# Kernel optimization log

Hardware: AMD Instinct MI355X
Metric: run time of the kernel (lower is better)

## Reference

```python
import jax, jax.numpy as jnp
import numpy as np

D_MODEL = 512; D_INNER = 1024; D_STATE = 16; D_CONV = 4; DT_RANK = 32
MRI_DIM = 1024; CLIN_DIM = 64; N_SLICES = 2000; CHUNK = 500; N_LAYERS = 3; N_HEADS = 8


def _ln(x, g, b, eps=1e-5):
    m = x.mean(-1, keepdims=True)
    v = ((x - m) ** 2).mean(-1, keepdims=True)
    return (x - m) / jnp.sqrt(v + eps) * g + b


def _mamba(x, in_proj, conv_w, conv_b, x_proj, dt_w, dt_b, A_log, Dp, out_proj):
    # x: (B, L, d_model). Faithful mamba-ssm block (no biases on in/out proj).
    B, L, _ = x.shape
    xz = jnp.einsum('bld,ed->ble', x, in_proj)          # (B, L, 2*d_inner)
    xr, z = jnp.split(xz, 2, axis=-1)
    # depthwise causal conv1d, kernel D_CONV, truncated to seqlen
    xp = jnp.pad(xr, ((0, 0), (D_CONV - 1, 0), (0, 0)))
    xc = sum(conv_w[:, k] * xp[:, k:k + L, :] for k in range(D_CONV)) + conv_b
    xc = jax.nn.silu(xc)                                # (B, L, d_inner)
    proj = jnp.einsum('bld,ed->ble', xc, x_proj)        # (B, L, dt_rank+2*d_state)
    dt_in = proj[..., :DT_RANK]
    Bm = proj[..., DT_RANK:DT_RANK + D_STATE]
    Cm = proj[..., DT_RANK + D_STATE:]
    dt = jax.nn.softplus(jnp.einsum('blr,dr->bld', dt_in, dt_w) + dt_b)  # (B, L, d_inner)
    A = -jnp.exp(A_log)                                 # (d_inner, d_state)
    dA = jnp.exp(dt[..., None] * A)                     # (B, L, d_inner, d_state)
    dBx = dt[..., None] * Bm[:, :, None, :] * xc[..., None]

    def step(h, inp):
        dA_t, dBx_t, C_t = inp
        h = dA_t * h + dBx_t
        return h, jnp.einsum('bds,bs->bd', h, C_t)

    h0 = jnp.zeros((B, D_INNER, D_STATE), x.dtype)
    _, ys = jax.lax.scan(step, h0, (dA.transpose(1, 0, 2, 3), dBx.transpose(1, 0, 2, 3), Cm.transpose(1, 0, 2)))
    y = ys.transpose(1, 0, 2) + Dp * xc
    y = y * jax.nn.silu(z)
    return jnp.einsum('ble,de->bld', y, out_proj)


def _mha(q, k, v, in_w, in_b, out_w, out_b, nh):
    # torch nn.MultiheadAttention (batch_first), returns (out, head-averaged weights)
    E = q.shape[-1]; hd = E // nh
    wq, wk, wv = jnp.split(in_w, 3, axis=0)
    bq, bk, bv = jnp.split(in_b, 3, axis=0)
    Q = (q @ wq.T + bq).reshape(q.shape[0], q.shape[1], nh, hd)
    K = (k @ wk.T + bk).reshape(k.shape[0], k.shape[1], nh, hd)
    V = (v @ wv.T + bv).reshape(v.shape[0], v.shape[1], nh, hd)
    s = jnp.einsum('blhd,bshd->bhls', Q, K) / jnp.sqrt(jnp.asarray(hd, q.dtype))
    a = jax.nn.softmax(s, axis=-1)
    o = jnp.einsum('bhls,bshd->blhd', a, V).reshape(q.shape[0], q.shape[1], E)
    return o @ out_w.T + out_b, a.mean(axis=1)


def setup_inputs() -> dict:
    key = jax.random.key(0)
    ks = iter(jax.random.split(key, 100))
    def rnd(shape, s=0.02):
        return s * jax.random.normal(next(ks), shape, jnp.float32)
    d = {}
    d['slice_features'] = jax.random.normal(next(ks), (N_SLICES, MRI_DIM), jnp.float32)
    d['clinical_features'] = jax.random.normal(next(ks), (CLIN_DIM,), jnp.float32)
    d['enc_in_W'] = rnd((D_MODEL, MRI_DIM)); d['enc_in_b'] = jnp.zeros((D_MODEL,))
    d['enc_in_ln_g'] = jnp.ones((D_MODEL,)); d['enc_in_ln_b'] = jnp.zeros((D_MODEL,))
    def mamba_params(n):
        return dict(
            in_proj=rnd((n, 2 * D_INNER, D_MODEL)),
            conv_w=rnd((n, D_INNER, D_CONV), 0.1),
            conv_b=jnp.zeros((n, D_INNER)),
            x_proj=rnd((n, DT_RANK + 2 * D_STATE, D_INNER)),
            dt_w=rnd((n, D_INNER, DT_RANK), 0.1),
            dt_b=jnp.full((n, D_INNER), -4.6, jnp.float32),  # softplus ~ 0.01
            A_log=jnp.log(jnp.broadcast_to(jnp.arange(1, D_STATE + 1, dtype=jnp.float32), (n, D_INNER, D_STATE))),
            D=jnp.ones((n, D_INNER)),
            out_proj=rnd((n, D_MODEL, D_INNER)))
    for k2, v in mamba_params(2).items():
        d['em_' + k2] = v
    d['enc_ln_g'] = jnp.ones((2, D_MODEL)); d['enc_ln_b'] = jnp.zeros((2, D_MODEL))
    d['enc_out_W'] = rnd((D_MODEL, D_MODEL)); d['enc_out_b'] = jnp.zeros((D_MODEL,))
    d['cl_w1'] = rnd((64, CLIN_DIM)); d['cl_b1'] = jnp.zeros((64,))
    d['cl_ln1_g'] = jnp.ones((64,)); d['cl_ln1_b'] = jnp.zeros((64,))
    d['cl_w2'] = rnd((D_MODEL, 64)); d['cl_b2'] = jnp.zeros((D_MODEL,))
    d['cl_ln2_g'] = jnp.ones((D_MODEL,)); d['cl_ln2_b'] = jnp.zeros((D_MODEL,))
    for k2, v in mamba_params(N_LAYERS).items():
        d['lm_' + k2] = v
    d['l_mln_g'] = jnp.ones((N_LAYERS, D_MODEL)); d['l_mln_b'] = jnp.zeros((N_LAYERS, D_MODEL))
    d['ca_in_w'] = rnd((N_LAYERS, 3 * D_MODEL, D_MODEL)); d['ca_in_b'] = jnp.zeros((N_LAYERS, 3 * D_MODEL))
    d['ca_out_w'] = rnd((N_LAYERS, D_MODEL, D_MODEL)); d['ca_out_b'] = jnp.zeros((N_LAYERS, D_MODEL))
    d['ca_ln_g'] = jnp.ones((N_LAYERS, D_MODEL)); d['ca_ln_b'] = jnp.zeros((N_LAYERS, D_MODEL))
    d['ff_w1'] = rnd((N_LAYERS, 2 * D_MODEL, D_MODEL)); d['ff_b1'] = jnp.zeros((N_LAYERS, 2 * D_MODEL))
    d['ff_w2'] = rnd((N_LAYERS, D_MODEL, 2 * D_MODEL)); d['ff_b2'] = jnp.zeros((N_LAYERS, D_MODEL))
    d['ffn_ln_g'] = jnp.ones((N_LAYERS, D_MODEL)); d['ffn_ln_b'] = jnp.zeros((N_LAYERS, D_MODEL))
    d['agg_in_w'] = rnd((3 * D_MODEL, D_MODEL)); d['agg_in_b'] = jnp.zeros((3 * D_MODEL,))
    d['agg_out_w'] = rnd((D_MODEL, D_MODEL)); d['agg_out_b'] = jnp.zeros((D_MODEL,))
    d['op_w'] = rnd((64, D_MODEL)); d['op_b'] = jnp.zeros((64,))
    d['op_ln_g'] = jnp.ones((64,)); d['op_ln_b'] = jnp.zeros((64,))
    return d


def reference(slice_features, clinical_features, enc_in_W, enc_in_b, enc_in_ln_g, enc_in_ln_b,
              em_in_proj, em_conv_w, em_conv_b, em_x_proj, em_dt_w, em_dt_b, em_A_log, em_D, em_out_proj,
              enc_ln_g, enc_ln_b, enc_out_W, enc_out_b,
              cl_w1, cl_b1, cl_ln1_g, cl_ln1_b, cl_w2, cl_b2, cl_ln2_g, cl_ln2_b,
              lm_in_proj, lm_conv_w, lm_conv_b, lm_x_proj, lm_dt_w, lm_dt_b, lm_A_log, lm_D, lm_out_proj,
              l_mln_g, l_mln_b, ca_in_w, ca_in_b, ca_out_w, ca_out_b, ca_ln_g, ca_ln_b,
              ff_w1, ff_b1, ff_w2, ff_b2, ffn_ln_g, ffn_ln_b,
              agg_in_w, agg_in_b, agg_out_w, agg_out_b, op_w, op_b, op_ln_g, op_ln_b):
    # --- MRI slice encoder: chunks of 500 slices, each a Mamba sequence (batched over chunks) ---
    h = slice_features.reshape(N_SLICES // CHUNK, CHUNK, MRI_DIM)
    h = _ln(h @ enc_in_W.T + enc_in_b, enc_in_ln_g, enc_in_ln_b)
    for i in range(2):
        res = h
        h = _mamba(h, em_in_proj[i], em_conv_w[i], em_conv_b[i], em_x_proj[i],
                   em_dt_w[i], em_dt_b[i], em_A_log[i], em_D[i], em_out_proj[i])
        h = _ln(h + res, enc_ln_g[i], enc_ln_b[i])
    mri = (h @ enc_out_W.T + enc_out_b).reshape(N_SLICES, D_MODEL)
    mri = jax.lax.stop_gradient(mri)  # .detach() in the original
    # --- clinical encoder ---
    c = jax.nn.relu(_ln(cl_w1 @ clinical_features + cl_b1, cl_ln1_g, cl_ln1_b))
    c = jax.nn.relu(_ln(cl_w2 @ c + cl_b2, cl_ln2_g, cl_ln2_b))
    seq = mri[None]                 # (1, N, D)
    cseq = c.reshape(1, 1, D_MODEL)
    # --- MambaFormer cross-attention layers ---
    for i in range(N_LAYERS):
        res = seq
        m = _mamba(seq, lm_in_proj[i], lm_conv_w[i], lm_conv_b[i], lm_x_proj[i],
                   lm_dt_w[i], lm_dt_b[i], lm_A_log[i], lm_D[i], lm_out_proj[i])
        seq = _ln(m + res, l_mln_g[i], l_mln_b[i])
        att, _ = _mha(seq, cseq, cseq, ca_in_w[i], ca_in_b[i], ca_out_w[i], ca_out_b[i], N_HEADS)
        seq = _ln(att + seq, ca_ln_g[i], ca_ln_b[i])
        f = jax.nn.gelu(seq @ ff_w1[i].T + ff_b1[i], approximate=False) @ ff_w2[i].T + ff_b2[i]
        seq = _ln(f + seq, ffn_ln_g[i], ffn_ln_b[i])
    # --- attention aggregation ---
    agg, w = _mha(seq, seq, seq, agg_in_w, agg_in_b, agg_out_w, agg_out_b, N_HEADS)
    scores = w.mean(axis=1)[0]                      # (N,): mean over query dim of head-avg weights
    emb = jnp.sum(scores[:, None] * agg[0], axis=0)  # (D,)
    return jax.nn.relu(_ln(op_w @ emb + op_b, op_ln_g, op_ln_b))
```

## Files before the change

kernel.cpp:

```cpp
#include <hip/hip_runtime.h>
#include <hip/hip_bf16.h>

#define NSL 2000
#define DM 512
#define DI 1024
#define DS 16
#define DTR 32

enum {
  IN_SLICE=0, IN_CLIN, IN_ENC_IN_W, IN_ENC_IN_B, IN_ENC_IN_LN_G, IN_ENC_IN_LN_B,
  IN_EM_IN_PROJ, IN_EM_CONV_W, IN_EM_CONV_B, IN_EM_X_PROJ, IN_EM_DT_W, IN_EM_DT_B,
  IN_EM_A_LOG, IN_EM_D, IN_EM_OUT_PROJ, IN_ENC_LN_G, IN_ENC_LN_B, IN_ENC_OUT_W, IN_ENC_OUT_B,
  IN_CL_W1, IN_CL_B1, IN_CL_LN1_G, IN_CL_LN1_B, IN_CL_W2, IN_CL_B2, IN_CL_LN2_G, IN_CL_LN2_B,
  IN_LM_IN_PROJ, IN_LM_CONV_W, IN_LM_CONV_B, IN_LM_X_PROJ, IN_LM_DT_W, IN_LM_DT_B,
  IN_LM_A_LOG, IN_LM_D, IN_LM_OUT_PROJ, IN_L_MLN_G, IN_L_MLN_B,
  IN_CA_IN_W, IN_CA_IN_B, IN_CA_OUT_W, IN_CA_OUT_B, IN_CA_LN_G, IN_CA_LN_B,
  IN_FF_W1, IN_FF_B1, IN_FF_W2, IN_FF_B2, IN_FFN_LN_G, IN_FFN_LN_B,
  IN_AGG_IN_W, IN_AGG_IN_B, IN_AGG_OUT_W, IN_AGG_OUT_B,
  IN_OP_W, IN_OP_B, IN_OP_LN_G, IN_OP_LN_B
};

typedef __attribute__((ext_vector_type(8))) __bf16 bf16x8;
typedef __attribute__((ext_vector_type(4))) float f32x4;
typedef __attribute__((ext_vector_type(8))) unsigned short u16x8;

__device__ __forceinline__ float softplusf_(float x) {
  return (x > 15.f) ? x : __logf(1.f + __expf(x));
}
__device__ __forceinline__ float siluf_(float x) {
  return x / (1.f + __expf(-x));
}
__device__ __forceinline__ unsigned short f2bf(float f) {
  unsigned int u = __float_as_uint(f);
  u += 0x7fff + ((u >> 16) & 1);
  return (unsigned short)(u >> 16);
}

#define NCVT 13
struct CvtArgs {
  const float* s[NCVT];
  unsigned short* d[NCVT];
  int n[NCVT];
};
__global__ __launch_bounds__(256) void cvt_batch(CvtArgs a) {
  const int ti = blockIdx.y;
  const int base = (blockIdx.x * 256 + threadIdx.x) * 16;
  if (base >= a.n[ti]) return;
  const float* s = a.s[ti];
  unsigned short* d = a.d[ti];
#pragma unroll
  for (int q = 0; q < 4; ++q) {
    float4 v = *reinterpret_cast<const float4*>(s + base + q * 4);
    ushort4 u; u.x = f2bf(v.x); u.y = f2bf(v.y); u.z = f2bf(v.z); u.w = f2bf(v.w);
    *reinterpret_cast<ushort4*>(d + base + q * 4) = u;
  }
}

template<int BM, int BN, int EPI>
__global__ __launch_bounds__(256) void gemm_mfma(
    const unsigned short* __restrict__ A, int lda,
    const unsigned short* __restrict__ W, int ldw,
    const float* __restrict__ bias,
    float* __restrict__ C, unsigned short* __restrict__ C16, int ldc,
    int M, int N, int K)
{
  constexpr int LS = 72;
  __shared__ unsigned short Als[BM][LS];
  __shared__ unsigned short Wls[BN][LS];
  constexpr int TPRA = 256 / BM;
  constexpr int USA  = 64 / TPRA;
  constexpr int TPRW = 256 / BN;
  constexpr int USW  = 64 / TPRW;
  constexpr int FM = BM / 32, FN = BN / 32;

  const int tid  = threadIdx.x;
  const int m0   = blockIdx.y * BM, n0 = blockIdx.x * BN;
  const int wave = tid >> 6, lane = tid & 63;
  const int wm   = wave >> 1, wn = wave & 1;
  const int lrow = lane & 15, lgrp = lane >> 4;

  f32x4 acc[FM][FN];
#pragma unroll
  for (int i = 0; i < FM; ++i)
#pragma unroll
    for (int j = 0; j < FN; ++j) acc[i][j] = (f32x4){0.f, 0.f, 0.f, 0.f};

  const int sra = tid / TPRA, ska = (tid % TPRA) * USA;
  const int srw = tid / TPRW, skw = (tid % TPRW) * USW;
  const int gma = m0 + sra;
  const int gnw = n0 + srw;

  for (int k0 = 0; k0 < K; k0 += 64) {
#pragma unroll
    for (int f = 0; f < USA / 8; ++f) {
      u16x8 v = {0,0,0,0,0,0,0,0};
      if (gma < M) v = *reinterpret_cast<const u16x8*>(&A[(size_t)gma * lda + k0 + ska + 8 * f]);
      *reinterpret_cast<u16x8*>(&Als[sra][ska + 8 * f]) = v;
    }
#pragma unroll
    for (int f = 0; f < USW / 8; ++f) {
      u16x8 v = {0,0,0,0,0,0,0,0};
      if (gnw < N) v = *reinterpret_cast<const u16x8*>(&W[(size_t)gnw * ldw + k0 + skw + 8 * f]);
      *reinterpret_cast<u16x8*>(&Wls[srw][skw + 8 * f]) = v;
    }
    __syncthreads();
#pragma unroll
    for (int ks = 0; ks < 2; ++ks) {
      bf16x8 am[FM], bn[FN];
#pragma unroll
      for (int i = 0; i < FM; ++i)
        am[i] = *reinterpret_cast<const bf16x8*>(&Als[wm * (BM / 2) + i * 16 + lrow][ks * 32 + lgrp * 8]);
#pragma unroll
      for (int j = 0; j < FN; ++j)
        bn[j] = *reinterpret_cast<const bf16x8*>(&Wls[wn * (BN / 2) + j * 16 + lrow][ks * 32 + lgrp * 8]);
#pragma unroll
      for (int i = 0; i < FM; ++i)
#pragma unroll
        for (int j = 0; j < FN; ++j)
          acc[i][j] = __builtin_amdgcn_mfma_f32_16x16x32_bf16(am[i], bn[j], acc[i][j], 0, 0, 0);
    }
    __syncthreads();
  }

#pragma unroll
  for (int i = 0; i < FM; ++i) {
#pragma unroll
    for (int j = 0; j < FN; ++j) {
#pragma unroll
      for (int q = 0; q < 4; ++q) {
        int gm = m0 + wm * (BM / 2) + i * 16 + lgrp * 4 + q;
        int gn = n0 + wn * (BN / 2) + j * 16 + lrow;
        if (gm < M && gn < N) {
          float v = acc[i][j][q];
          if (bias) v += bias[gn];
          if (EPI == 1) v = 0.5f * v * (1.f + erff(v * 0.70710678118654752f));
          if (C)   C[(size_t)gm * ldc + gn] = v;
          if (C16) C16[(size_t)gm * ldc + gn] = f2bf(v);
        }
      }
    }
  }
}

__global__ __launch_bounds__(256) void ln512_kernel(
    const float* __restrict__ x, const float* __restrict__ res,
    const float* __restrict__ g, const float* __restrict__ b,
    float* __restrict__ out, unsigned short* __restrict__ out16)
{
  const int row = blockIdx.x, tid = threadIdx.x;
  const size_t base = (size_t)row * 512;
  float v0 = x[base + tid], v1 = x[base + tid + 256];
  if (res) { v0 += res[base + tid];  v1 += res[base + tid + 256]; }
  float s = v0 + v1, ss = v0*v0 + v1*v1;
#pragma unroll
  for (int off = 1; off < 64; off <<= 1) {
    s  += __shfl_xor(s,  off);
    ss += __shfl_xor(ss, off);
  }
  __shared__ float rs[4], rss[4];
  int wid = tid >> 6, lane = tid & 63;
  if (lane == 0) { rs[wid] = s; rss[wid] = ss; }
  __syncthreads();
  s  = rs[0] + rs[1] + rs[2] + rs[3];
  ss = rss[0] + rss[1] + rss[2] + rss[3];
  float mean = s * (1.f/512.f);
  float var  = ss * (1.f/512.f) - mean*mean;
  float rstd = rsqrtf(var + 1e-5f);
  float o0 = g[tid]     * (v0 - mean) * rstd + b[tid];
  float o1 = g[tid+256] * (v1 - mean) * rstd + b[tid+256];
  out[base + tid]       = o0;
  out[base + tid + 256] = o1;
  if (out16) {
    out16[base + tid]       = f2bf(o0);
    out16[base + tid + 256] = f2bf(o1);
  }
}

__global__ __launch_bounds__(256) void ln512_dual(
    const float* __restrict__ x, const float* __restrict__ res,
    const float* __restrict__ addvec,
    const float* __restrict__ g1, const float* __restrict__ b1,
    const float* __restrict__ g2, const float* __restrict__ b2,
    float* __restrict__ out, unsigned short* __restrict__ out16)
{
  const int row = blockIdx.x, tid = threadIdx.x;
  const size_t base = (size_t)row * 512;
  __shared__ float rs[4], rss[4];
  int wid = tid >> 6, lane = tid & 63;

  float v0 = x[base + tid] + res[base + tid];
  float v1 = x[base + tid + 256] + res[base + tid + 256];
  float s = v0 + v1, ss = v0*v0 + v1*v1;
#pragma unroll
  for (int off = 1; off < 64; off <<= 1) { s += __shfl_xor(s, off); ss += __shfl_xor(ss, off); }
  if (lane == 0) { rs[wid] = s; rss[wid] = ss; }
  __syncthreads();
  s  = rs[0] + rs[1] + rs[2] + rs[3];
  ss = rss[0] + rss[1] + rss[2] + rss[3];
  float mean = s * (1.f/512.f);
  float rstd = rsqrtf(ss * (1.f/512.f) - mean*mean + 1e-5f);
  float u0 = g1[tid]     * (v0 - mean) * rstd + b1[tid]     + addvec[tid];
  float u1 = g1[tid+256] * (v1 - mean) * rstd + b1[tid+256] + addvec[tid+256];

  float s2 = u0 + u1, ss2 = u0*u0 + u1*u1;
#pragma unroll
  for (int off = 1; off < 64; off <<= 1) { s2 += __shfl_xor(s2, off); ss2 += __shfl_xor(ss2, off); }
  __syncthreads();
  if (lane == 0) { rs[wid] = s2; rss[wid] = ss2; }
  __syncthreads();
  s2  = rs[0] + rs[1] + rs[2] + rs[3];
  ss2 = rss[0] + rss[1] + rss[2] + rss[3];
  float mean2 = s2 * (1.f/512.f);
  float rstd2 = rsqrtf(ss2 * (1.f/512.f) - mean2*mean2 + 1e-5f);
  float o0 = g2[tid]     * (u0 - mean2) * rstd2 + b2[tid];
  float o1 = g2[tid+256] * (u1 - mean2) * rstd2 + b2[tid+256];
  out[base + tid]       = o0;
  out[base + tid + 256] = o1;
  out16[base + tid]       = f2bf(o0);
  out16[base + tid + 256] = f2bf(o1);
}

__global__ __launch_bounds__(256) void conv_silu_kernel(
    const float* __restrict__ xz, const float* __restrict__ cw,
    const float* __restrict__ cb, float* __restrict__ xc,
    unsigned short* __restrict__ xc16, int L)
{
  int idx = blockIdx.x * 256 + threadIdx.x;
  if (idx >= NSL * DI) return;
  int rrow = idx >> 10, c = idx & 1023;
  int l = rrow % L;
  float acc = cb[c];
  const float w0 = cw[c*4+0], w1 = cw[c*4+1], w2 = cw[c*4+2], w3 = cw[c*4+3];
  const float* base = xz + (size_t)rrow * 2048 + c;
  if (l >= 3) acc += w0 * base[-3*2048];
  if (l >= 2) acc += w1 * base[-2*2048];
  if (l >= 1) acc += w2 * base[-1*2048];
  acc += w3 * base[0];
  float r = siluf_(acc);
  xc[idx] = r;
  xc16[idx] = f2bf(r);
}

__global__ __launch_bounds__(256) void scan_p1(
    const float* __restrict__ proj, const float* __restrict__ dt_w,
    const float* __restrict__ dt_b, const float* __restrict__ xc,
    float* __restrict__ Pb, float* __restrict__ Eb, int L, int T)
{
  const int lane = threadIdx.x & 63, wave = threadIdx.x >> 6;
  const int dl = wave * 32 + (lane & 31);
  const int shalf = lane >> 5;
  const int d = blockIdx.x * 128 + dl;
  const int c = blockIdx.y, b = blockIdx.z, B = gridDim.z;
  const int s0 = shalf * 8;

  float dtw[32];
#pragma unroll
  for (int q = 0; q < 8; ++q)
    *reinterpret_cast<float4*>(&dtw[q*4]) = *reinterpret_cast<const float4*>(&dt_w[(size_t)d * 32 + q * 4]);
  const float dtbv = dt_b[d];

  float h[8];
#pragma unroll
  for (int s = 0; s < 8; ++s) h[s] = 0.f;
  float R = 1.f;

  int t0 = c * T, t1 = t0 + T; if (t1 > L) t1 = L;
  for (int t = t0; t < t1; ++t) {
    size_t row = (size_t)b * L + t;
    const float* pr = proj + row * 64;
    float dacc = dtbv;
#pragma unroll
    for (int q = 0; q < 8; ++q) {
      float4 p4 = *reinterpret_cast<const float4*>(pr + q * 4);
      dacc = fmaf(p4.x, dtw[q*4+0], dacc);
      dacc = fmaf(p4.y, dtw[q*4+1], dacc);
      dacc = fmaf(p4.z, dtw[q*4+2], dacc);
      dacc = fmaf(p4.w, dtw[q*4+3], dacc);
    }
    float dtv = softplusf_(dacc);
    float r1 = __expf(-dtv);
    float xcv = xc[row * 1024 + d];
    float u = dtv * xcv;
    float4 b0 = *reinterpret_cast<const float4*>(pr + 32 + s0);
    float4 b1 = *reinterpret_cast<const float4*>(pr + 36 + s0);
    float r2 = r1 * r1, r4 = r2 * r2, r8 = r4 * r4;
    float rp = shalf ? (r8 * r1) : r1;
    h[0] = fmaf(rp, h[0], u * b0.x); rp *= r1;
    h[1] = fmaf(rp, h[1], u * b0.y); rp *= r1;
    h[2] = fmaf(rp, h[2], u * b0.z); rp *= r1;
    h[3] = fmaf(rp, h[3], u * b0.w); rp *= r1;
    h[4] = fmaf(rp, h[4], u * b1.x); rp *= r1;
    h[5] = fmaf(rp, h[5], u * b1.y); rp *= r1;
    h[6] = fmaf(rp, h[6], u * b1.z); rp *= r1;
    h[7] = fmaf(rp, h[7], u * b1.w);
    R *= r1;
  }
  float R2 = R * R, R4 = R2 * R2, R8 = R4 * R4;
  float Rp = shalf ? (R8 * R) : R;
  float P[8];
  P[0] = Rp; Rp *= R; P[1] = Rp; Rp *= R; P[2] = Rp; Rp *= R; P[3] = Rp; Rp *= R;
  P[4] = Rp; Rp *= R; P[5] = Rp; Rp *= R; P[6] = Rp; Rp *= R; P[7] = Rp;
  size_t o = (((size_t)(c * B + b)) << 14) + (size_t)d * 16 + s0;
  *reinterpret_cast<float4*>(&Pb[o])     = (float4){P[0], P[1], P[2], P[3]};
  *reinterpret_cast<float4*>(&Pb[o + 4]) = (float4){P[4], P[5], P[6], P[7]};
  *reinterpret_cast<float4*>(&Eb[o])     = (float4){h[0], h[1], h[2], h[3]};
  *reinterpret_cast<float4*>(&Eb[o + 4]) = (float4){h[4], h[5], h[6], h[7]};
}

__global__ __launch_bounds__(256) void scan_comb(
    const float* __restrict__ Pb, const float* __restrict__ Eb,
    float* __restrict__ Gb, int B, int nC)
{
  int idx = blockIdx.x * 256 + threadIdx.x;
  if (idx >= B * 16384) return;
  int b = idx >> 14, ds = idx & 16383;
  float gacc = 0.f;
#pragma unroll 4
  for (int c = 0; c < nC; ++c) {
    size_t o = (((size_t)(c * B + b)) << 14) + ds;
    Gb[o] = gacc;
    gacc = fmaf(Pb[o], gacc, Eb[o]);
  }
}

__global__ __launch_bounds__(256) void scan_p3(
    const float* __restrict__ proj, const float* __restrict__ dt_w,
    const float* __restrict__ dt_b, const float* __restrict__ xc,
    const float* __restrict__ xz, const float* __restrict__ Dp,
    const float* __restrict__ Gb, unsigned short* __restrict__ y16, int L, int T)
{
  const int lane = threadIdx.x & 63, wave = threadIdx.x >> 6;
  const int dl = wave * 32 + (lane & 31);
  const int shalf = lane >> 5;
  const int d = blockIdx.x * 128 + dl;
  const int c = blockIdx.y, b = blockIdx.z, B = gridDim.z;
  const int s0 = shalf * 8;

  float dtw[32];
#pragma unroll
  for (int q = 0; q < 8; ++q)
    *reinterpret_cast<float4*>(&dtw[q*4]) = *reinterpret_cast<const float4*>(&dt_w[(size_t)d * 32 + q * 4]);
  const float dtbv = dt_b[d];
  const float Dv = Dp[d];

  size_t o = (((size_t)(c * B + b)) << 14) + (size_t)d * 16 + s0;
  float4 g0 = *reinterpret_cast<const float4*>(&Gb[o]);
  float4 g1 = *reinterpret_cast<const float4*>(&Gb[o + 4]);
  float h[8] = {g0.x, g0.y, g0.z, g0.w, g1.x, g1.y, g1.z, g1.w};

  int t0 = c * T, t1 = t0 + T; if (t1 > L) t1 = L;
  for (int t = t0; t < t1; ++t) {
    size_t row = (size_t)b * L + t;
    const float* pr = proj + row * 64;
    float dacc = dtbv;
#pragma unroll
    for (int q = 0; q < 8; ++q) {
      float4 p4 = *reinterpret_cast<const float4*>(pr + q * 4);
      dacc = fmaf(p4.x, dtw[q*4+0], dacc);
      dacc = fmaf(p4.y, dtw[q*4+1], dacc);
      dacc = fmaf(p4.z, dtw[q*4+2], dacc);
      dacc = fmaf(p4.w, dtw[q*4+3], dacc);
    }
    float dtv = softplusf_(dacc);
    float r1 = __expf(-dtv);
    float xcv = xc[row * 1024 + d];
    float u = dtv * xcv;
    float4 b0 = *reinterpret_cast<const float4*>(pr + 32 + s0);
    float4 b1 = *reinterpret_cast<const float4*>(pr + 36 + s0);
    float4 c0 = *reinterpret_cast<const float4*>(pr + 48 + s0);
    float4 c1 = *reinterpret_cast<const float4*>(pr + 52 + s0);
    float r2 = r1 * r1, r4 = r2 * r2, r8 = r4 * r4;
    float rp = shalf ? (r8 * r1) : r1;
    float yv;
    h[0] = fmaf(rp, h[0], u * b0.x); yv  = h[0] * c0.x; rp *= r1;
    h[1] = fmaf(rp, h[1], u * b0.y); yv = fmaf(h[1], c0.y, yv); rp *= r1;
    h[2] = fmaf(rp, h[2], u * b0.z); yv = fmaf(h[2], c0.z, yv); rp *= r1;
    h[3] = fmaf(rp, h[3], u * b0.w); yv = fmaf(h[3], c0.w, yv); rp *= r1;
    h[4] = fmaf(rp, h[4], u * b1.x); yv = fmaf(h[4], c1.x, yv); rp *= r1;
    h[5] = fmaf(rp, h[5], u * b1.y); yv = fmaf(h[5], c1.y, yv); rp *= r1;
    h[6] = fmaf(rp, h[6], u * b1.z); yv = fmaf(h[6], c1.z, yv); rp *= r1;
    h[7] = fmaf(rp, h[7], u * b1.w); yv = fmaf(h[7], c1.w, yv);
    yv += __shfl_xor(yv, 32);
    if (shalf == 0) {
      float zv = xz[row * 2048 + 1024 + d];
      y16[row * 1024 + d] = f2bf((yv + Dv * xcv) * siluf_(zv));
    }
  }
}

__global__ __launch_bounds__(512) void clinical_kernel(
    const float* __restrict__ clin,
    const float* __restrict__ w1, const float* __restrict__ b1,
    const float* __restrict__ g1, const float* __restrict__ bb1,
    const float* __restrict__ w2, const float* __restrict__ b2,
    const float* __restrict__ g2, const float* __restrict__ bb2,
    float* __restrict__ c2out)
{
  __shared__ float cs[64], c1[64], red[16];
  const int tid = threadIdx.x;
  if (tid < 64) cs[tid] = clin[tid];
  __syncthreads();
  if (tid < 64) {
    float a1 = b1[tid];
    for (int k = 0; k < 64; ++k) a1 = fmaf(w1[tid*64 + k], cs[k], a1);
    float s = a1, ss = a1*a1;
#pragma unroll
    for (int off = 1; off < 64; off <<= 1) { s += __shfl_xor(s, off); ss += __shfl_xor(ss, off); }
    float m = s * (1.f/64.f), var = ss * (1.f/64.f) - m*m;
    float r = rsqrtf(var + 1e-5f);
    float v = g1[tid] * (a1 - m) * r + bb1[tid];
    c1[tid] = fmaxf(v, 0.f);
  }
  __syncthreads();
  float a2 = b2[tid];
  for (int k = 0; k < 64; ++k) a2 = fmaf(w2[tid*64 + k], c1[k], a2);
  float s = a2, ss = a2*a2;
#pragma unroll
  for (int off = 1; off < 64; off <<= 1) { s += __shfl_xor(s, off); ss += __shfl_xor(ss, off); }
  int wid = tid >> 6, lane = tid & 63;
  if (lane == 0) { red[wid] = s; red[8 + wid] = ss; }
  __syncthreads();
  s = 0.f; ss = 0.f;
#pragma unroll
  for (int q = 0; q < 8; ++q) { s += red[q]; ss += red[8+q]; }
  float m = s * (1.f/512.f), var = ss * (1.f/512.f) - m*m;
  float r = rsqrtf(var + 1e-5f);
  c2out[tid] = fmaxf(g2[tid] * (a2 - m) * r + bb2[tid], 0.f);
}

__global__ __launch_bounds__(256) void attvec_v(
    const float* __restrict__ c2, const float* __restrict__ ca_in_w,
    const float* __restrict__ ca_in_b, float* __restrict__ vsb)
{
  const int layer = blockIdx.y;
  const int wave = threadIdx.x >> 6, lane = threadIdx.x & 63;
  const int n = blockIdx.x * 4 + wave;
  const float* wr = ca_in_w + (size_t)layer * 1536 * 512 + (size_t)(1024 + n) * 512 + lane * 8;
  const float* xr = c2 + lane * 8;
  float4 w0 = *reinterpret_cast<const float4*>(wr);
  float4 w1 = *reinterpret_cast<const float4*>(wr + 4);
  float4 x0 = *reinterpret_cast<const float4*>(xr);
  float4 x1 = *reinterpret_cast<const float4*>(xr + 4);
  float acc = w0.x*x0.x + w0.y*x0.y + w0.z*x0.z + w0.w*x0.w
            + w1.x*x1.x + w1.y*x1.y + w1.z*x1.z + w1.w*x1.w;
#pragma unroll
  for (int off = 1; off < 64; off <<= 1) acc += __shfl_xor(acc, off);
  if (lane == 0) vsb[layer * 512 + n] = acc + ca_in_b[layer * 1536 + 1024 + n];
}
__global__ __launch_bounds__(256) void attvec_o(
    const float* __restrict__ vsb, const float* __restrict__ ca_out_w,
    const float* __restrict__ ca_out_b, float* __restrict__ attvec)
{
  const int layer = blockIdx.y;
  const int wave = threadIdx.x >> 6, lane = threadIdx.x & 63;
  const int n = blockIdx.x * 4 + wave;
  const float* wr = ca_out_w + (size_t)layer * 512 * 512 + (size_t)n * 512 + lane * 8;
  const float* xr = vsb + layer * 512 + lane * 8;
  float4 w0 = *reinterpret_cast<const float4*>(wr);
  float4 w1 = *reinterpret_cast<const float4*>(wr + 4);
  float4 x0 = *reinterpret_cast<const float4*>(xr);
  float4 x1 = *reinterpret_cast<const float4*>(xr + 4);
  float acc = w0.x*x0.x + w0.y*x0.y + w0.z*x0.z + w0.w*x0.w
            + w1.x*x1.x + w1.y*x1.y + w1.z*x1.z + w1.w*x1.w;
#pragma unroll
  for (int off = 1; off < 64; off <<= 1) acc += __shfl_xor(acc, off);
  if (lane == 0) attvec[layer * 512 + n] = acc + ca_out_b[layer * 512 + n];
}

__global__ __launch_bounds__(256) void vt_build(
    const unsigned short* __restrict__ qkv16, unsigned short* __restrict__ vtg)
{
  __shared__ unsigned short Ls[64][68];
  const int tid = threadIdx.x;
  const int kb = blockIdx.x, h = blockIdx.y;
#pragma unroll
  for (int i = 0; i < 4; ++i) {
    int idx = i * 256 + tid;
    int kl = idx >> 4, d4 = idx & 15;
    int key = kb * 64 + kl;
    ushort4 v = {0, 0, 0, 0};
    if (key < NSL) v = *reinterpret_cast<const ushort4*>(&qkv16[(size_t)key * 1536 + 1024 + h * 64 + d4 * 4]);
    *reinterpret_cast<ushort4*>(&Ls[kl][d4 * 4]) = v;
  }
  __syncthreads();
#pragma unroll
  for (int i = 0; i < 16; ++i) {
    int idx = i * 256 + tid;
    int d = idx >> 6, kl = idx & 63;
    vtg[(((size_t)h * 64 + d) << 11) + kb * 64 + kl] = Ls[kl][d];
  }
}

__global__ __launch_bounds__(256) void attn_stats_mfma(
    const unsigned short* __restrict__ qkv16, float* __restrict__ rowZinv)
{
  __shared__ unsigned short Qs[64][72];
  __shared__ unsigned short Ks[128][72];
  const int tid = threadIdx.x;
  const int h = blockIdx.y, l0 = blockIdx.x * 64;
  const int wave = tid >> 6, lane = tid & 63;
  const int lr = lane & 15, lg = lane >> 4;
  {
    int ql = tid >> 2, dh = (tid & 3) * 16;
    int gq = l0 + ql;
#pragma unroll
    for (int j = 0; j < 2; ++j) {
      u16x8 v = {0,0,0,0,0,0,0,0};
      if (gq < NSL) v = *reinterpret_cast<const u16x8*>(&qkv16[(size_t)gq * 1536 + h * 64 + dh + 8 * j]);
      *reinterpret_cast<u16x8*>(&Qs[ql][dh + 8 * j]) = v;
    }
  }
  float Z[4] = {0.f, 0.f, 0.f, 0.f};

  for (int kt = 0; kt < NSL; kt += 128) {
    __syncthreads();
    {
      int kl = tid >> 1, dh = (tid & 1) * 32;
      int gk = kt + kl;
#pragma unroll
      for (int j = 0; j < 4; ++j) {
        u16x8 v = {0,0,0,0,0,0,0,0};
        if (gk < NSL) v = *reinterpret_cast<const u16x8*>(&qkv16[(size_t)gk * 1536 + 512 + h * 64 + dh + 8 * j]);
        *reinterpret_cast<u16x8*>(&Ks[kl][dh + 8 * j]) = v;
      }
    }
    __syncthreads();
    f32x4 acc[8];
#pragma unroll
    for (int f = 0; f < 8; ++f) acc[f] = (f32x4){0.f, 0.f, 0.f, 0.f};
#pragma unroll
    for (int ks = 0; ks < 2; ++ks) {
      bf16x8 a = *reinterpret_cast<const bf16x8*>(&Qs[wave * 16 + lr][ks * 32 + lg * 8]);
#pragma unroll
      for (int f = 0; f < 8; ++f) {
        bf16x8 b = *reinterpret_cast<const bf16x8*>(&Ks[f * 16 + lr][ks * 32 + lg * 8]);
        acc[f] = __builtin_amdgcn_mfma_f32_16x16x32_bf16(a, b, acc[f], 0, 0, 0);
      }
    }
#pragma unroll
    for (int q = 0; q < 4; ++q) {
      float se = 0.f;
#pragma unroll
      for (int f = 0; f < 8; ++f) {
        int key = kt + f * 16 + lr;
        if (key < NSL) se += __expf(acc[f][q] * 0.125f);
      }
#pragma unroll
      for (int off = 1; off < 16; off <<= 1) se += __shfl_xor(se, off);
      Z[q] += se;
    }
  }
  if (lr == 0) {
#pragma unroll
    for (int q = 0; q < 4; ++q) {
      int row = l0 + wave * 16 + lg * 4 + q;
      if (row < NSL) rowZinv[h * NSL + row] = 1.f / Z[q];
    }
  }
}

__global__ __launch_bounds__(256) void attn_av_mfma(
    const unsigned short* __restrict__ qkv16, const unsigned short* __restrict__ vtg,
    const float* __restrict__ rowZinv,
    unsigned short* __restrict__ Obuf16, float* __restrict__ colsum)
{
  __shared__ unsigned short Qs[64][72];
  __shared__ unsigned short Ks[128][72];
  __shared__ unsigned short Vts[64][136];
  __shared__ unsigned short Ps[64][136];
  __shared__ float colacc[128];
  const int tid = threadIdx.x;
  const int h = blockIdx.y, l0 = blockIdx.x * 64;
  const int wave = tid >> 6, lane = tid & 63;
  const int lr = lane & 15, lg = lane >> 4;
  {
    int ql = tid >> 2, dh = (tid & 3) * 16;
    int gq = l0 + ql;
#pragma unroll
    for (int j = 0; j < 2; ++j) {
      u16x8 v = {0,0,0,0,0,0,0,0};
      if (gq < NSL) v = *reinterpret_cast<const u16x8*>(&qkv16[(size_t)gq * 1536 + h * 64 + dh + 8 * j]);
      *reinterpret_cast<u16x8*>(&Qs[ql][dh + 8 * j]) = v;
    }
  }
  if (tid < 128) colacc[tid] = 0.f;
  float zi[4];
#pragma unroll
  for (int q = 0; q < 4; ++q) {
    int row = l0 + wave * 16 + lg * 4 + q;
    zi[q] = (row < NSL) ? rowZinv[h * NSL + row] : 0.f;
  }
  f32x4 oacc[4];
#pragma unroll
  for (int df = 0; df < 4; ++df) oacc[df] = (f32x4){0.f, 0.f, 0.f, 0.f};

  for (int kt = 0; kt < NSL; kt += 128) {
    __syncthreads();
    {
      int kl = tid >> 1, dh = (tid & 1) * 32;
      int gk = kt + kl;
#pragma unroll
      for (int j = 0; j < 4; ++j) {
        u16x8 v = {0,0,0,0,0,0,0,0};
        if (gk < NSL) v = *reinterpret_cast<const u16x8*>(&qkv16[(size_t)gk * 1536 + 512 + h * 64 + dh + 8 * j]);
        *reinterpret_cast<u16x8*>(&Ks[kl][dh + 8 * j]) = v;
      }
    }
    {
      int d = tid >> 2, kq = (tid & 3) * 32;
#pragma unroll
      for (int j = 0; j < 4; ++j) {
        u16x8 v = *reinterpret_cast<const u16x8*>(&vtg[(((size_t)h * 64 + d) << 11) + kt + kq + 8 * j]);
        *reinterpret_cast<u16x8*>(&Vts[d][kq + 8 * j]) = v;
      }
    }
    __syncthreads();
    f32x4 acc[8];
#pragma unroll
    for (int f = 0; f < 8; ++f) acc[f] = (f32x4){0.f, 0.f, 0.f, 0.f};
#pragma unroll
    for (int ks = 0; ks < 2; ++ks) {
      bf16x8 a = *reinterpret_cast<const bf16x8*>(&Qs[wave * 16 + lr][ks * 32 + lg * 8]);
#pragma unroll
      for (int f = 0; f < 8; ++f) {
        bf16x8 b = *reinterpret_cast<const bf16x8*>(&Ks[f * 16 + lr][ks * 32 + lg * 8]);
        acc[f] = __builtin_amdgcn_mfma_f32_16x16x32_bf16(a, b, acc[f], 0, 0, 0);
      }
    }
#pragma unroll
    for (int f = 0; f < 8; ++f) {
      float csum = 0.f;
#pragma unroll
      for (int q = 0; q < 4; ++q) {
        int key = kt + f * 16 + lr;
        float p = (key < NSL) ? __expf(acc[f][q] * 0.125f) * zi[q] : 0.f;
        Ps[wave * 16 + lg * 4 + q][f * 16 + lr] = f2bf(p);
        csum += p;
      }
      csum += __shfl_xor(csum, 16);
      csum += __shfl_xor(csum, 32);
      if (lane < 16) atomicAdd(&colacc[f * 16 + lr], csum);
    }
    __syncthreads();
#pragma unroll
    for (int ks = 0; ks < 4; ++ks) {
      bf16x8 pa = *reinterpret_cast<const bf16x8*>(&Ps[wave * 16 + lr][ks * 32 + lg * 8]);
#pragma unroll
      for (int df = 0; df < 4; ++df) {
        bf16x8 vb = *reinterpret_cast<const bf16x8*>(&Vts[df * 16 + lr][ks * 32 + lg * 8]);
        oacc[df] = __builtin_amdgcn_mfma_f32_16x16x32_bf16(pa, vb, oacc[df], 0, 0, 0);
      }
    }
    if (tid < 128) {
      int key = kt + tid;
      if (key < NSL) atomicAdd(&colsum[key], colacc[tid]);
      colacc[tid] = 0.f;
    }
  }
#pragma unroll
  for (int df = 0; df < 4; ++df) {
#pragma unroll
    for (int q = 0; q < 4; ++q) {
      int row = l0 + wave * 16 + lg * 4 + q;
      if (row < NSL) Obuf16[(size_t)row * 512 + h * 64 + df * 16 + lr] = f2bf(oacc[df][q]);
    }
  }
}

__global__ __launch_bounds__(256) void wsum_kernel(
    const float* __restrict__ agg, const float* __restrict__ colsum,
    float* __restrict__ emb)
{
  int d = blockIdx.x * 256 + threadIdx.x;
  int l0 = blockIdx.y * 125, l1 = l0 + 125;
  float acc = 0.f;
  for (int l = l0; l < l1; ++l) acc = fmaf(colsum[l], agg[(size_t)l*512 + d], acc);
  atomicAdd(&emb[d], acc * (1.f / 16000.f));
}

__global__ __launch_bounds__(512) void final_kernel(
    const float* __restrict__ emb, const float* __restrict__ opw,
    const float* __restrict__ opb, const float* __restrict__ g,
    const float* __restrict__ b, float* __restrict__ out)
{
  const int tid = threadIdx.x;
  const int n = tid >> 3, sub = tid & 7;
  const float* wr = opw + (size_t)n * 512 + sub * 64;
  const float* er = emb + sub * 64;
  float acc = 0.f;
#pragma unroll
  for (int k = 0; k < 64; k += 4) {
    float4 w4 = *reinterpret_cast<const float4*>(wr + k);
    float4 e4 = *reinterpret_cast<const float4*>(er + k);
    acc = fmaf(w4.x, e4.x, acc); acc = fmaf(w4.y, e4.y, acc);
    acc = fmaf(w4.z, e4.z, acc); acc = fmaf(w4.w, e4.w, acc);
  }
  acc += __shfl_xor(acc, 1);
  acc += __shfl_xor(acc, 2);
  acc += __shfl_xor(acc, 4);
  __shared__ float av[64];
  if (sub == 0) av[n] = acc + opb[n];
  __syncthreads();
  if (tid < 64) {
    float a = av[tid];
    float s = a, ss = a * a;
#pragma unroll
    for (int off = 1; off < 64; off <<= 1) { s += __shfl_xor(s, off); ss += __shfl_xor(ss, off); }
    float mean = s * (1.f/64.f), var = ss * (1.f/64.f) - mean*mean;
    float r = rsqrtf(var + 1e-5f);
    out[tid] = fmaxf(g[tid] * (a - mean) * r + b[tid], 0.f);
  }
}

extern "C" void kernel_launch(void* const* d_in, const int* in_sizes, int n_in,
                              void* d_out, int out_size, void* d_ws, size_t ws_size,
                              hipStream_t stream)
{
  (void)in_sizes; (void)n_in; (void)out_size; (void)ws_size;
  const float* IN[58];
  for (int i = 0; i < 58; ++i) IN[i] = (const float*)d_in[i];

  float* w = (float*)d_ws;
  float* s0     = w + 0;
  float* s1     = w + 1024000;
  float* xz     = w + 2048000;
  float* xc     = w + 6144000;
  float* projb  = w + 8192000;
  float* Pb     = w + 8320000;
  float* Eb     = w + 9958400;
  float* Gb     = w + 11596800;
  float* rowZ   = w + 13251200;
  float* colsum = w + 13267200;
  float* c2     = w + 13269200;
  float* vsb    = w + 13269712;
  float* attvec = w + 13271248;
  float* emb    = w + 13272784;

  unsigned short* U = (unsigned short*)(w + 13400000);
  unsigned short* slice16 = U + 0;
  unsigned short* s0b     = U + 2048000;
  unsigned short* s1b     = U + 3072000;
  unsigned short* xc16    = U + 4096000;
  unsigned short* y16     = U + 6144000;
  unsigned short* ob16    = U + 8192000;
  unsigned short* enc_in_w16   = U + 9216000;
  unsigned short* em_in_proj16 = U + 9740288;
  unsigned short* em_x_proj16  = U + 11837440;
  unsigned short* em_out_proj16= U + 11968512;
  unsigned short* enc_out_w16  = U + 13017088;
  unsigned short* lm_in_proj16 = U + 13279232;
  unsigned short* lm_x_proj16  = U + 16424960;
  unsigned short* lm_out_proj16= U + 16621568;
  unsigned short* ff_w1_16     = U + 18194432;
  unsigned short* ff_w2_16     = U + 19767296;
  unsigned short* agg_in_w16   = U + 21340160;
  unsigned short* agg_out_w16  = U + 22126592;

  unsigned short* qkv16 = (unsigned short*)xz;
  unsigned short* vtg   = (unsigned short*)(xz + 2000000);

  CvtArgs ca;
  ca.s[0]=IN[IN_SLICE];      ca.d[0]=slice16;        ca.n[0]=2048000;
  ca.s[1]=IN[IN_ENC_IN_W];   ca.d[1]=enc_in_w16;     ca.n[1]=524288;
  ca.s[2]=IN[IN_EM_IN_PROJ]; ca.d[2]=em_in_proj16;   ca.n[2]=2097152;
  ca.s[3]=IN[IN_EM_X_PROJ];  ca.d[3]=em_x_proj16;    ca.n[3]=131072;
  ca.s[4]=IN[IN_EM_OUT_PROJ];ca.d[4]=em_out_proj16;  ca.n[4]=1048576;
  ca.s[5]=IN[IN_ENC_OUT_W];  ca.d[5]=enc_out_w16;    ca.n[5]=262144;
  ca.s[6]=IN[IN_LM_IN_PROJ]; ca.d[6]=lm_in_proj16;   ca.n[6]=3145728;
  ca.s[7]=IN[IN_LM_X_PROJ];  ca.d[7]=lm_x_proj16;    ca.n[7]=196608;
  ca.s[8]=IN[IN_LM_OUT_PROJ];ca.d[8]=lm_out_proj16;  ca.n[8]=1572864;
  ca.s[9]=IN[IN_FF_W1];      ca.d[9]=ff_w1_16;       ca.n[9]=1572864;
  ca.s[10]=IN[IN_FF_W2];     ca.d[10]=ff_w2_16;      ca.n[10]=1572864;
  ca.s[11]=IN[IN_AGG_IN_W];  ca.d[11]=agg_in_w16;    ca.n[11]=786432;
  ca.s[12]=IN[IN_AGG_OUT_W]; ca.d[12]=agg_out_w16;   ca.n[12]=262144;
  cvt_batch<<<dim3(768, NCVT), 256, 0, stream>>>(ca);

  clinical_kernel<<<1, 512, 0, stream>>>(IN[IN_CLIN], IN[IN_CL_W1], IN[IN_CL_B1],
      IN[IN_CL_LN1_G], IN[IN_CL_LN1_B], IN[IN_CL_W2], IN[IN_CL_B2],
      IN[IN_CL_LN2_G], IN[IN_CL_LN2_B], c2);
  attvec_v<<<dim3(128, 3), 256, 0, stream>>>(c2, IN[IN_CA_IN_W], IN[IN_CA_IN_B], vsb);
  attvec_o<<<dim3(128, 3), 256, 0, stream>>>(vsb, IN[IN_CA_OUT_W], IN[IN_CA_OUT_B], attvec);

  const dim3 blk(256);
  const int MT128 = (NSL + 127) / 128;
  const int MT64  = (NSL + 63) / 64;

  gemm_mfma<64,64,0><<<dim3(8, MT64), blk, 0, stream>>>(slice16, 1024, enc_in_w16, 1024,
      IN[IN_ENC_IN_B], s1, nullptr, 512, NSL, 512, 1024);
  ln512_kernel<<<NSL, blk, 0, stream>>>(s1, nullptr, IN[IN_ENC_IN_LN_G], IN[IN_ENC_IN_LN_B], s0, s0b);

  auto run_mamba = [&](const unsigned short* xin16, float* mout,
                       const unsigned short* in_proj16, const float* conv_w, const float* conv_b,
                       const unsigned short* x_proj16, const float* dt_w, const float* dt_b,
                       const float* Dp, const unsigned short* out_proj16,
                       int B, int L) {
    const int M = B * L;
    const int T = 20, nC = (L + T - 1) / T;
    gemm_mfma<128,128,0><<<dim3(16, MT128), blk, 0, stream>>>(xin16, 512, in_proj16, 512, nullptr, xz, nullptr, 2048, M, 2048, 512);
    conv_silu_kernel<<<(M*1024 + 255)/256, blk, 0, stream>>>(xz, conv_w, conv_b, xc, xc16, L);
    gemm_mfma<64,64,0><<<dim3(1, MT64), blk, 0, stream>>>(xc16, 1024, x_proj16, 1024, nullptr, projb, nullptr, 64, M, 64, 1024);
    scan_p1<<<dim3(8, nC, B), blk, 0, stream>>>(projb, dt_w, dt_b, xc, Pb, Eb, L, T);
    scan_comb<<<(B*16384 + 255)/256, blk, 0, stream>>>(Pb, Eb, Gb, B, nC);
    scan_p3<<<dim3(8, nC, B), blk, 0, stream>>>(projb, dt_w, dt_b, xc, xz, Dp, Gb, y16, L, T);
    gemm_mfma<64,64,0><<<dim3(8, MT64), blk, 0, stream>>>(y16, 1024, out_proj16, 1024, nullptr, mout, nullptr, 512, M, 512, 1024);
  };

  for (int i = 0; i < 2; ++i) {
    run_mamba(s0b, s1,
        em_in_proj16 + (size_t)i*1048576, IN[IN_EM_CONV_W] + i*4096, IN[IN_EM_CONV_B] + i*1024,
        em_x_proj16 + i*65536, IN[IN_EM_DT_W] + i*32768, IN[IN_EM_DT_B] + i*1024,
        IN[IN_EM_D] + i*1024, em_out_proj16 + (size_t)i*524288,
        4, 500);
    ln512_kernel<<<NSL, blk, 0, stream>>>(s1, s0, IN[IN_ENC_LN_G] + i*512, IN[IN_ENC_LN_B] + i*512, s0, s0b);
  }
  gemm_mfma<64,64,0><<<dim3(8, MT64), blk, 0, stream>>>(s0b, 512, enc_out_w16, 512,
      IN[IN_ENC_OUT_B], s1, s1b, 512, NSL, 512, 512);

  for (int i = 0; i < 3; ++i) {
    run_mamba(s1b, s0,
        lm_in_proj16 + (size_t)i*1048576, IN[IN_LM_CONV_W] + i*4096, IN[IN_LM_CONV_B] + i*1024,
        lm_x_proj16 + i*65536, IN[IN_LM_DT_W] + i*32768, IN[IN_LM_DT_B] + i*1024,
        IN[IN_LM_D] + i*1024, lm_out_proj16 + (size_t)i*524288,
        1, 2000);
    ln512_dual<<<NSL, blk, 0, stream>>>(s0, s1, attvec + i*512,
        IN[IN_L_MLN_G] + i*512, IN[IN_L_MLN_B] + i*512,
        IN[IN_CA_LN_G] + i*512, IN[IN_CA_LN_B] + i*512, s1, s1b);
    gemm_mfma<128,128,1><<<dim3(8, MT128), blk, 0, stream>>>(s1b, 512, ff_w1_16 + (size_t)i*524288, 512,
        IN[IN_FF_B1] + i*1024, nullptr, xc16, 1024, NSL, 1024, 512);
    gemm_mfma<64,64,0><<<dim3(8, MT64), blk, 0, stream>>>(xc16, 1024, ff_w2_16 + (size_t)i*524288, 1024,
        IN[IN_FF_B2] + i*512, s0, nullptr, 512, NSL, 512, 1024);
    ln512_kernel<<<NSL, blk, 0, stream>>>(s0, s1, IN[IN_FFN_LN_G] + i*512, IN[IN_FFN_LN_B] + i*512, s1, s1b);
  }

  gemm_mfma<128,128,0><<<dim3(12, MT128), blk, 0, stream>>>(s1b, 512, agg_in_w16, 512,
      IN[IN_AGG_IN_B], nullptr, qkv16, 1536, NSL, 1536, 512);
  vt_build<<<dim3(32, 8), blk, 0, stream>>>(qkv16, vtg);
  hipMemsetAsync(colsum, 0, NSL * sizeof(float), stream);
  hipMemsetAsync(emb, 0, 512 * sizeof(float), stream);
  attn_stats_mfma<<<dim3(32, 8), blk, 0, stream>>>(qkv16, rowZ);
  attn_av_mfma<<<dim3(32, 8), blk, 0, stream>>>(qkv16, vtg, rowZ, ob16, colsum);
  gemm_mfma<64,64,0><<<dim3(8, MT64), blk, 0, stream>>>(ob16, 512, agg_out_w16, 512,
      IN[IN_AGG_OUT_B], s0, nullptr, 512, NSL, 512, 512);
  wsum_kernel<<<dim3(2, 16), blk, 0, stream>>>(s0, colsum, emb);
  final_kernel<<<1, 512, 0, stream>>>(emb, IN[IN_OP_W], IN[IN_OP_B],
      IN[IN_OP_LN_G], IN[IN_OP_LN_B], (float*)d_out);
}
```

Before: 1.100 ms.

## Split attention over keys and use 64x128 GEMM tiles for more blocks

The aggregation attention stats and AV kernels now split the key range across a new grid z-dimension of two. Partial row sums and partial outputs are combined with atomic adds into zeroed buffers, and new kernels invert the row sums and convert the fp32 output to bf16. Several large GEMMs also switch from 128x128 to 64x128 tiles to launch more workgroups and improve occupancy on the many-CU GPU. The cost is extra memsets, atomics and small kernels. The split boundary at 1000 is not aligned to the 128-key tile, so the kt loop in the second half reads tiles starting at 1000, which is handled by kend masking.

```diff
diff --git a/kernel.cpp b/kernel.cpp
--- a/kernel.cpp
+++ b/kernel.cpp
@@ -6,6 +6,7 @@
 #define DI 1024
 #define DS 16
 #define DTR 32
+#define KVSPLIT 2
 
 enum {
   IN_SLICE=0, IN_CLIN, IN_ENC_IN_W, IN_ENC_IN_B, IN_ENC_IN_LN_G, IN_ENC_IN_LN_B,
@@ -54,6 +55,24 @@
     ushort4 u; u.x = f2bf(v.x); u.y = f2bf(v.y); u.z = f2bf(v.z); u.w = f2bf(v.w);
     *reinterpret_cast<ushort4*>(d + base + q * 4) = u;
   }
+}
+
+__global__ __launch_bounds__(256) void cvt_f2b(
+    const float* __restrict__ s, unsigned short* __restrict__ d, int n)
+{
+  int i = (blockIdx.x * 256 + threadIdx.x) * 8;
+  if (i >= n) return;
+  float4 a = *reinterpret_cast<const float4*>(s + i);
+  float4 b = *reinterpret_cast<const float4*>(s + i + 4);
+  ushort4 u0; u0.x = f2bf(a.x); u0.y = f2bf(a.y); u0.z = f2bf(a.z); u0.w = f2bf(a.w);
+  ushort4 u1; u1.x = f2bf(b.x); u1.y = f2bf(b.y); u1.z = f2bf(b.z); u1.w = f2bf(b.w);
+  *reinterpret_cast<ushort4*>(d + i)     = u0;
+  *reinterpret_cast<ushort4*>(d + i + 4) = u1;
+}
+
+__global__ __launch_bounds__(256) void inv_kernel(float* __restrict__ z, int n) {
+  int i = blockIdx.x * 256 + threadIdx.x;
+  if (i < n) z[i] = 1.f / z[i];
 }
 
 template<int BM, int BN, int EPI>
@@ -492,12 +511,14 @@
 }
 
 __global__ __launch_bounds__(256) void attn_stats_mfma(
-    const unsigned short* __restrict__ qkv16, float* __restrict__ rowZinv)
+    const unsigned short* __restrict__ qkv16, float* __restrict__ rowZ)
 {
   __shared__ unsigned short Qs[64][72];
   __shared__ unsigned short Ks[128][72];
   const int tid = threadIdx.x;
   const int h = blockIdx.y, l0 = blockIdx.x * 64;
+  const int kbeg = blockIdx.z * (NSL / KVSPLIT);
+  const int kend = kbeg + NSL / KVSPLIT;
   const int wave = tid >> 6, lane = tid & 63;
   const int lr = lane & 15, lg = lane >> 4;
   {
@@ -512,7 +533,7 @@
   }
   float Z[4] = {0.f, 0.f, 0.f, 0.f};
 
-  for (int kt = 0; kt < NSL; kt += 128) {
+  for (int kt = kbeg; kt < kend; kt += 128) {
     __syncthreads();
     {
       int kl = tid >> 1, dh = (tid & 1) * 32;
@@ -543,7 +564,7 @@
 #pragma unroll
       for (int f = 0; f < 8; ++f) {
         int key = kt + f * 16 + lr;
-        if (key < NSL) se += __expf(acc[f][q] * 0.125f);
+        if (key < kend) se += __expf(acc[f][q] * 0.125f);
       }
 #pragma unroll
       for (int off = 1; off < 16; off <<= 1) se += __shfl_xor(se, off);
@@ -554,7 +575,7 @@
 #pragma unroll
     for (int q = 0; q < 4; ++q) {
       int row = l0 + wave * 16 + lg * 4 + q;
-      if (row < NSL) rowZinv[h * NSL + row] = 1.f / Z[q];
+      if (row < NSL) atomicAdd(&rowZ[h * NSL + row], Z[q]);
     }
   }
 }
@@ -562,7 +583,7 @@
 __global__ __launch_bounds__(256) void attn_av_mfma(
     const unsigned short* __restrict__ qkv16, const unsigned short* __restrict__ vtg,
     const float* __restrict__ rowZinv,
-    unsigned short* __restrict__ Obuf16, float* __restrict__ colsum)
+    float* __restrict__ ObufF, float* __restrict__ colsum)
 {
   __shared__ unsigned short Qs[64][72];
   __shared__ unsigned short Ks[128][72];
@@ -571,6 +592,8 @@
   __shared__ float colacc[128];
   const int tid = threadIdx.x;
   const int h = blockIdx.y, l0 = blockIdx.x * 64;
+  const int kbeg = blockIdx.z * (NSL / KVSPLIT);
+  const int kend = kbeg + NSL / KVSPLIT;
   const int wave = tid >> 6, lane = tid & 63;
   const int lr = lane & 15, lg = lane >> 4;
   {
@@ -594,7 +617,7 @@
 #pragma unroll
   for (int df = 0; df < 4; ++df) oacc[df] = (f32x4){0.f, 0.f, 0.f, 0.f};
 
-  for (int kt = 0; kt < NSL; kt += 128) {
+  for (int kt = kbeg; kt < kend; kt += 128) {
     __syncthreads();
     {
       int kl = tid >> 1, dh = (tid & 1) * 32;
@@ -610,7 +633,9 @@
       int d = tid >> 2, kq = (tid & 3) * 32;
 #pragma unroll
       for (int j = 0; j < 4; ++j) {
-        u16x8 v = *reinterpret_cast<const u16x8*>(&vtg[(((size_t)h * 64 + d) << 11) + kt + kq + 8 * j]);
+        int key = kt + kq + 8 * j;
+        u16x8 v = {0,0,0,0,0,0,0,0};
+        if (key < NSL) v = *reinterpret_cast<const u16x8*>(&vtg[(((size_t)h * 64 + d) << 11) + key]);
         *reinterpret_cast<u16x8*>(&Vts[d][kq + 8 * j]) = v;
       }
     }
@@ -633,7 +658,7 @@
 #pragma unroll
       for (int q = 0; q < 4; ++q) {
         int key = kt + f * 16 + lr;
-        float p = (key < NSL) ? __expf(acc[f][q] * 0.125f) * zi[q] : 0.f;
+        float p = (key < kend) ? __expf(acc[f][q] * 0.125f) * zi[q] : 0.f;
         Ps[wave * 16 + lg * 4 + q][f * 16 + lr] = f2bf(p);
         csum += p;
       }
@@ -653,7 +678,7 @@
     }
     if (tid < 128) {
       int key = kt + tid;
-      if (key < NSL) atomicAdd(&colsum[key], colacc[tid]);
+      if (key < kend) atomicAdd(&colsum[key], colacc[tid]);
       colacc[tid] = 0.f;
     }
   }
@@ -662,7 +687,7 @@
 #pragma unroll
     for (int q = 0; q < 4; ++q) {
       int row = l0 + wave * 16 + lg * 4 + q;
-      if (row < NSL) Obuf16[(size_t)row * 512 + h * 64 + df * 16 + lr] = f2bf(oacc[df][q]);
+      if (row < NSL) atomicAdd(&ObufF[(size_t)row * 512 + h * 64 + df * 16 + lr], oacc[df][q]);
     }
   }
 }
@@ -758,6 +783,7 @@
 
   unsigned short* qkv16 = (unsigned short*)xz;
   unsigned short* vtg   = (unsigned short*)(xz + 2000000);
+  float* obufF = xc;
 
   CvtArgs ca;
   ca.s[0]=IN[IN_SLICE];      ca.d[0]=slice16;        ca.n[0]=2048000;
@@ -796,7 +822,7 @@
                        int B, int L) {
     const int M = B * L;
     const int T = 20, nC = (L + T - 1) / T;
-    gemm_mfma<128,128,0><<<dim3(16, MT128), blk, 0, stream>>>(xin16, 512, in_proj16, 512, nullptr, xz, nullptr, 2048, M, 2048, 512);
+    gemm_mfma<64,128,0><<<dim3(16, MT64), blk, 0, stream>>>(xin16, 512, in_proj16, 512, nullptr, xz, nullptr, 2048, M, 2048, 512);
     conv_silu_kernel<<<(M*1024 + 255)/256, blk, 0, stream>>>(xz, conv_w, conv_b, xc, xc16, L);
     gemm_mfma<64,64,0><<<dim3(1, MT64), blk, 0, stream>>>(xc16, 1024, x_proj16, 1024, nullptr, projb, nullptr, 64, M, 64, 1024);
     scan_p1<<<dim3(8, nC, B), blk, 0, stream>>>(projb, dt_w, dt_b, xc, Pb, Eb, L, T);
@@ -825,20 +851,24 @@
     ln512_dual<<<NSL, blk, 0, stream>>>(s0, s1, attvec + i*512,
         IN[IN_L_MLN_G] + i*512, IN[IN_L_MLN_B] + i*512,
         IN[IN_CA_LN_G] + i*512, IN[IN_CA_LN_B] + i*512, s1, s1b);
-    gemm_mfma<128,128,1><<<dim3(8, MT128), blk, 0, stream>>>(s1b, 512, ff_w1_16 + (size_t)i*524288, 512,
+    gemm_mfma<64,128,1><<<dim3(8, MT64), blk, 0, stream>>>(s1b, 512, ff_w1_16 + (size_t)i*524288, 512,
         IN[IN_FF_B1] + i*1024, nullptr, xc16, 1024, NSL, 1024, 512);
     gemm_mfma<64,64,0><<<dim3(8, MT64), blk, 0, stream>>>(xc16, 1024, ff_w2_16 + (size_t)i*524288, 1024,
         IN[IN_FF_B2] + i*512, s0, nullptr, 512, NSL, 512, 1024);
     ln512_kernel<<<NSL, blk, 0, stream>>>(s0, s1, IN[IN_FFN_LN_G] + i*512, IN[IN_FFN_LN_B] + i*512, s1, s1b);
   }
 
-  gemm_mfma<128,128,0><<<dim3(12, MT128), blk, 0, stream>>>(s1b, 512, agg_in_w16, 512,
+  gemm_mfma<64,128,0><<<dim3(12, MT64), blk, 0, stream>>>(s1b, 512, agg_in_w16, 512,
       IN[IN_AGG_IN_B], nullptr, qkv16, 1536, NSL, 1536, 512);
   vt_build<<<dim3(32, 8), blk, 0, stream>>>(qkv16, vtg);
+  hipMemsetAsync(rowZ, 0, 8 * NSL * sizeof(float), stream);
   hipMemsetAsync(colsum, 0, NSL * sizeof(float), stream);
   hipMemsetAsync(emb, 0, 512 * sizeof(float), stream);
-  attn_stats_mfma<<<dim3(32, 8), blk, 0, stream>>>(qkv16, rowZ);
-  attn_av_mfma<<<dim3(32, 8), blk, 0, stream>>>(qkv16, vtg, rowZ, ob16, colsum);
+  hipMemsetAsync(obufF, 0, (size_t)NSL * 512 * sizeof(float), stream);
+  attn_stats_mfma<<<dim3(32, 8, KVSPLIT), blk, 0, stream>>>(qkv16, rowZ);
+  inv_kernel<<<(8 * NSL + 255) / 256, blk, 0, stream>>>(rowZ, 8 * NSL);
+  attn_av_mfma<<<dim3(32, 8, KVSPLIT), blk, 0, stream>>>(qkv16, vtg, rowZ, obufF, colsum);
+  cvt_f2b<<<(NSL * 512 / 8 + 255) / 256, blk, 0, stream>>>(obufF, ob16, NSL * 512);
   gemm_mfma<64,64,0><<<dim3(8, MT64), blk, 0, stream>>>(ob16, 512, agg_out_w16, 512,
       IN[IN_AGG_OUT_B], s0, nullptr, 512, NSL, 512, 512);
   wsum_kernel<<<dim3(2, 16), blk, 0, stream>>>(s0, colsum, emb);
```

New measurement: 1.044 ms. 1.05x faster.
